# Kernel tuning notes

Hardware: AMD Instinct MI355X
Metric: run time of the kernel (lower is better)

Reference implementation:

```python
import jax, jax.numpy as jnp
import numpy as np

B, S, D = 4, 4096, 64
NEG = -1e9  # matches masked_fill(-1000000000.0)


def setup_inputs() -> dict:
    key = jax.random.key(0)
    ks = jax.random.split(key, 10)
    inp = {
        "E": jax.random.normal(ks[0], (B, S, D), jnp.float32),
        "P_K_emb": jax.random.normal(ks[1], (B, S, D), jnp.float32),
        "P_V_emb": jax.random.normal(ks[2], (B, S, D), jnp.float32),
        "Wq": jax.random.normal(ks[3], (D, D), jnp.float32) * (1.0 / np.sqrt(D)),
        "bq": jax.random.normal(ks[4], (D,), jnp.float32) * 0.02,
        "Wk": jax.random.normal(ks[5], (D, D), jnp.float32) * (1.0 / np.sqrt(D)),
        "bk": jax.random.normal(ks[6], (D,), jnp.float32) * 0.02,
        "Wv": jax.random.normal(ks[7], (D, D), jnp.float32) * (1.0 / np.sqrt(D)),
        "bv": jax.random.normal(ks[8], (D,), jnp.float32) * 0.02,
        "pad_mask": jax.random.randint(ks[9], (B, S), 0, 2).astype(jnp.bool_),
    }
    return inp


def reference(E, P_K_emb, P_V_emb, Wq, bq, Wk, bk, Wv, bv, pad_mask):
    d = E.shape[-1]
    # torch nn.Linear: y = x @ W.T + b
    Q = E @ Wq.T + bq                       # [B,S,D]
    K = E @ Wk.T + bk
    V = E @ Wv.T + bv
    K_p = K * P_K_emb                       # popularity-modulated keys
    V_p = V * P_V_emb                       # popularity-modulated values
    scores = jnp.einsum('bqd,bkd->bqk', Q, K_p) / jnp.sqrt(jnp.float32(d))  # [B,S,S]
    S_len = E.shape[1]
    causal = jnp.triu(jnp.ones((S_len, S_len), jnp.bool_), k=1)             # [S,S]
    mask = pad_mask[:, None, :] | causal[None, :, :]                        # [B,S,S]
    scores = jnp.where(mask, jnp.float32(NEG), scores)
    attn = jax.nn.softmax(scores, axis=-1)
    O_I = jnp.einsum('bqk,bkd->bqd', attn, V_p)  # [B,S,D]
    return O_I
```

## Files before the change

kernel.cpp:

```cpp
#include <hip/hip_runtime.h>
#include <hip/hip_bf16.h>

#define Bn 4
#define Sn 4096
#define Dn 64

typedef short          s16x8 __attribute__((ext_vector_type(8)));
typedef unsigned short u16x8 __attribute__((ext_vector_type(8)));
typedef float          f32x4 __attribute__((ext_vector_type(4)));

typedef __attribute__((address_space(1))) const void gas_void;
typedef __attribute__((address_space(3))) void       las_void;

__device__ __forceinline__ unsigned short f2bf(float f) {
    unsigned u = __float_as_uint(f);
    u = u + 0x7fffu + ((u >> 16) & 1u);
    return (unsigned short)(u >> 16);
}
__device__ __forceinline__ float bf2f(unsigned short h) {
    return __uint_as_float(((unsigned)h) << 16);
}
__device__ __forceinline__ unsigned long long pack4(float4 x) {
    return (unsigned long long)f2bf(x.x)
         | ((unsigned long long)f2bf(x.y) << 16)
         | ((unsigned long long)f2bf(x.z) << 32)
         | ((unsigned long long)f2bf(x.w) << 48);
}
__device__ __forceinline__ void gld16(const void* g, void* l) {
    __builtin_amdgcn_global_load_lds((gas_void*)g, (las_void*)l, 16, 0, 0);
}

__global__ void LPSAN_init_kernel(const unsigned char* pm, unsigned long long* padbits,
                                  float* meanVsum) {
    const int k = blockIdx.x, t = threadIdx.x;
    if (k == 8) { meanVsum[t] = 0.f; return; }

    __shared__ unsigned nzs;
    if (t == 0) nzs = 0u;
    __syncthreads();
    {
        const uint2* p2 = (const uint2*)(pm + k * 2048);
        uint2 x = p2[t];
        unsigned acc = (x.x & 0xFFFFFF00u) | (x.y & 0xFFFFFF00u);
        if (acc) atomicOr(&nzs, 1u);
    }
    __syncthreads();
    if (t >= 32) return;
    const int wi = k * 32 + t;
    unsigned long long bits = 0ull;
    if (nzs) {
        const uint4* p4 = (const uint4*)(pm + wi * 64);
        #pragma unroll
        for (int q = 0; q < 4; ++q) {
            uint4 x = p4[q];
            unsigned w[4] = { x.x, x.y, x.z, x.w };
            #pragma unroll
            for (int wj = 0; wj < 4; ++wj)
                #pragma unroll
                for (int bb = 0; bb < 4; ++bb)
                    bits |= (unsigned long long)(((w[wj] >> (8 * bb)) & 0xFFu) != 0u)
                            << (q * 16 + wj * 4 + bb);
        }
    } else {
        const uint4* p4 = (const uint4*)pm + wi * 16;
        #pragma unroll
        for (int q = 0; q < 16; ++q) {
            uint4 x = p4[q];
            bits |= (unsigned long long)(x.x != 0u) << (q * 4);
            bits |= (unsigned long long)(x.y != 0u) << (q * 4 + 1);
            bits |= (unsigned long long)(x.z != 0u) << (q * 4 + 2);
            bits |= (unsigned long long)(x.w != 0u) << (q * 4 + 3);
        }
    }
    padbits[wi] = bits;
}

__global__ void LPSAN_proj_kernel(
    const float* __restrict__ E, const float* __restrict__ PK, const float* __restrict__ PV,
    const float* __restrict__ Wq, const float* __restrict__ bq,
    const float* __restrict__ Wk, const float* __restrict__ bk,
    const float* __restrict__ Wv, const float* __restrict__ bv,
    unsigned short* __restrict__ Qb, unsigned short* __restrict__ Kb,
    unsigned short* __restrict__ Vt, float* __restrict__ meanVsum)
{
    __shared__ unsigned short Ebf[4096];
    __shared__ unsigned short Wbf[3][4096];
    __shared__ unsigned short Tbuf[64 * 72];

    const int t = threadIdx.x;
    const int r0 = blockIdx.x * 64;
    const int b  = r0 >> 12;
    const int s0 = r0 & (Sn - 1);
    const int w = t >> 6, lane = t & 63;
    const int fq = lane >> 4, fr = lane & 15;

    {
        const float4* Eg = (const float4*)(E + (size_t)r0 * 64);
        #pragma unroll
        for (int v = 0; v < 4; ++v) {
            int f = t + v * 256;
            float4 x = Eg[f];
            int row = f >> 4, c4 = f & 15;
            *(unsigned long long*)((char*)Ebf + row * 128 + ((c4 * 8) ^ ((row & 7) << 4))) = pack4(x);
        }
        #pragma unroll
        for (int m = 0; m < 3; ++m) {
            const float4* Wg = (const float4*)(m == 0 ? Wq : m == 1 ? Wk : Wv);
            #pragma unroll
            for (int v = 0; v < 4; ++v) {
                int f = t + v * 256;
                float4 x = Wg[f];
                int row = f >> 4, c4 = f & 15;
                *(unsigned long long*)((char*)Wbf[m] + row * 128 + ((c4 * 8) ^ ((row & 7) << 4))) = pack4(x);
            }
        }
    }
    __syncthreads();

    const int  arow = w * 16 + fr;
    const int  swz  = (fr & 7) << 4;
    const char* Ec = (const char*)Ebf;
    const s16x8 ea0 = *(const s16x8*)(Ec + arow * 128 + ((fq * 16) ^ swz));
    const s16x8 ea1 = *(const s16x8*)(Ec + arow * 128 + ((64 + fq * 16) ^ swz));

    const int sl0 = w * 16 + fq * 4;

    for (int m = 0; m < 3; ++m) {
        const char*  Wc   = (const char*)Wbf[m];
        const float* bias = (m == 0) ? bq : (m == 1) ? bk : bv;

        f32x4 acc[4];
        #pragma unroll
        for (int ct = 0; ct < 4; ++ct) {
            const int brow = ct * 16 + fr;
            s16x8 b0 = *(const s16x8*)(Wc + brow * 128 + ((fq * 16) ^ swz));
            s16x8 b1 = *(const s16x8*)(Wc + brow * 128 + ((64 + fq * 16) ^ swz));
            f32x4 z = f32x4{0.f, 0.f, 0.f, 0.f};
            z = __builtin_amdgcn_mfma_f32_16x16x32_bf16(ea0, b0, z, 0, 0, 0);
            z = __builtin_amdgcn_mfma_f32_16x16x32_bf16(ea1, b1, z, 0, 0, 0);
            acc[ct] = z;
        }

        if (m < 2) {
            #pragma unroll
            for (int ct = 0; ct < 4; ++ct) {
                const int j = ct * 16 + fr;
                const float bb = bias[j];
                if (m == 0) {
                    #pragma unroll
                    for (int r = 0; r < 4; ++r)
                        Tbuf[(sl0 + r) * 72 + j] = f2bf((acc[ct][r] + bb) * 0.125f);
                } else {
                    #pragma unroll
                    for (int r = 0; r < 4; ++r) {
                        float mod = PK[(size_t)(r0 + sl0 + r) * 64 + j];
                        Tbuf[(sl0 + r) * 72 + j] = f2bf((acc[ct][r] + bb) * mod);
                    }
                }
            }
            __syncthreads();
            {
                unsigned short* dst = (m == 0 ? Qb : Kb)
                    + (size_t)(b * Sn + s0 + (t >> 2)) * 64 + (t & 3) * 16;
                u16x8 o0 = *(const u16x8*)&Tbuf[(t >> 2) * 72 + (t & 3) * 16];
                u16x8 o1 = *(const u16x8*)&Tbuf[(t >> 2) * 72 + (t & 3) * 16 + 8];
                *(u16x8*)dst = o0;
                *(u16x8*)(dst + 8) = o1;
            }
            __syncthreads();
        } else {
            #pragma unroll
            for (int ct = 0; ct < 4; ++ct) {
                const int j = ct * 16 + fr;
                const float bb = bias[j];
                unsigned long long pk = 0;
                #pragma unroll
                for (int r = 0; r < 4; ++r) {
                    float mod = PV[(size_t)(r0 + sl0 + r) * 64 + j];
                    pk |= (unsigned long long)f2bf((acc[ct][r] + bb) * mod) << (16 * r);
                }
                *(unsigned long long*)&Tbuf[j * 72 + sl0] = pk;
            }
            __syncthreads();
            {
                const int d = t >> 2, seg = t & 3;
                u16x8 o0 = *(const u16x8*)&Tbuf[d * 72 + seg * 16];
                u16x8 o1 = *(const u16x8*)&Tbuf[d * 72 + seg * 16 + 8];
                unsigned short* dst = Vt + (size_t)(b * 64 + d) * Sn + s0 + seg * 16;
                *(u16x8*)dst = o0;
                *(u16x8*)(dst + 8) = o1;
                float s = 0.f;
                #pragma unroll
                for (int i = 0; i < 8; ++i) s += bf2f(o0[i]) + bf2f(o1[i]);
                s += __shfl_xor(s, 1);
                s += __shfl_xor(s, 2);
                if ((t & 3) == 0) atomicAdd(&meanVsum[b * 64 + d], s);
            }
        }
    }
}

__global__ void LPSAN_attn_kernel(
    const unsigned short* __restrict__ Qb, const unsigned short* __restrict__ Kb,
    const unsigned short* __restrict__ Vt, const unsigned long long* __restrict__ padbits,
    const float* __restrict__ meanVsum,
    float* __restrict__ Oacc, float* __restrict__ Lsum, float* __restrict__ out)
{
    __shared__ unsigned short Klds[2][4096];
    __shared__ unsigned short Vlds[2][4096];
    __shared__ unsigned short Plds[4][1024];

    int id = 287 - blockIdx.x, g = 0, base = 0;
    while (id >= base + 8 * (g + 1)) { base += 8 * (g + 1); ++g; }
    const int rel = id - base;
    const int qt = 8 * g + rel / (g + 1);
    const int c  = rel % (g + 1);

    const int b = blockIdx.y;
    const int q0 = qt * 64;
    const int t0 = c * 8;
    const int tcnt = min(8, qt + 1 - t0);
    const int tid = threadIdx.x;
    const int w = tid >> 6, lane = tid & 63;
    const int fq = lane >> 4, fr = lane & 15;
    const int qw = q0 + w * 16;

    const unsigned short* Kbase = Kb + b * (Sn * Dn);
    const unsigned short* Vbase = Vt + b * (Dn * Sn);

    const s16x8 qf0 = *(const s16x8*)(Qb + (b * Sn + qw + fr) * 64 + fq * 8);
    const s16x8 qf1 = *(const s16x8*)(Qb + (b * Sn + qw + fr) * 64 + 32 + fq * 8);

    s16x8 onesb;
    #pragma unroll
    for (int i = 0; i < 8; ++i) onesb[i] = (short)0x3F80;

    f32x4 Oa[4];
    f32x4 lacc = f32x4{0.f, 0.f, 0.f, 0.f};
    #pragma unroll
    for (int i = 0; i < 4; ++i) Oa[i] = f32x4{0.f, 0.f, 0.f, 0.f};

    char* Pw = (char*)&Plds[w][0];

    auto STAGE = [&](int kv0, int bufi) {
        #pragma unroll
        for (int cc = 0; cc < 2; ++cc) {
            int pos = w * 2048 + cc * 1024 + lane * 16;
            int row = pos >> 7;
            int cl  = (pos & 127) ^ ((row & 7) << 4);
            gld16(Kbase + (kv0 + row) * 64 + (cl >> 1),
                  (char*)&Klds[bufi][0] + w * 2048 + cc * 1024);
            gld16(Vbase + row * Sn + kv0 + (cl >> 1),
                  (char*)&Vlds[bufi][0] + w * 2048 + cc * 1024);
        }
    };

    auto COMPUTE = [&](int t, int bufi, bool causal) {
        const char* Kc = (const char*)&Klds[bufi][0];
        const char* Vc = (const char*)&Vlds[bufi][0];
        const int kv0 = t * 64;

        f32x4 sc[4];
        #pragma unroll
        for (int tl = 0; tl < 4; ++tl) {
            int row = tl * 16 + fr;
            int swz = (row & 7) << 4;
            s16x8 k0 = *(const s16x8*)(Kc + row * 128 + ((fq * 16) ^ swz));
            s16x8 k1 = *(const s16x8*)(Kc + row * 128 + ((64 + fq * 16) ^ swz));
            f32x4 z = f32x4{0.f, 0.f, 0.f, 0.f};
            z = __builtin_amdgcn_mfma_f32_16x16x32_bf16(qf0, k0, z, 0, 0, 0);
            z = __builtin_amdgcn_mfma_f32_16x16x32_bf16(qf1, k1, z, 0, 0, 0);
            sc[tl] = z;
        }

        const unsigned long long bits = padbits[b * 64 + t];
        #pragma unroll
        for (int tl = 0; tl < 4; ++tl) {
            const bool pad = (bits >> (tl * 16 + fr)) & 1ull;
            const int col = kv0 + tl * 16 + fr;
            #pragma unroll
            for (int r = 0; r < 4; ++r) {
                float p = __expf(sc[tl][r] - 16.0f);
                bool msk = pad || (causal && (col > (qw + fq * 4 + r)));
                sc[tl][r] = msk ? 0.f : p;
            }
        }

        #pragma unroll
        for (int tl = 0; tl < 4; ++tl) {
            #pragma unroll
            for (int r = 0; r < 4; ++r) {
                int prow = fq * 4 + r;
                int pcb = (tl * 16 + fr) * 2;
                *(unsigned short*)(Pw + prow * 128 + (pcb ^ ((prow & 7) << 4))) = f2bf(sc[tl][r]);
            }
        }
        asm volatile("s_waitcnt lgkmcnt(0)" ::: "memory");
        __builtin_amdgcn_sched_barrier(0);

        s16x8 pa0 = *(const s16x8*)(Pw + fr * 128 + ((fq * 16) ^ ((fr & 7) << 4)));
        s16x8 pa1 = *(const s16x8*)(Pw + fr * 128 + ((64 + fq * 16) ^ ((fr & 7) << 4)));
        lacc = __builtin_amdgcn_mfma_f32_16x16x32_bf16(pa0, onesb, lacc, 0, 0, 0);
        lacc = __builtin_amdgcn_mfma_f32_16x16x32_bf16(pa1, onesb, lacc, 0, 0, 0);
        #pragma unroll
        for (int dt = 0; dt < 4; ++dt) {
            int row = dt * 16 + fr;
            int swz = (row & 7) << 4;
            s16x8 v0 = *(const s16x8*)(Vc + row * 128 + ((fq * 16) ^ swz));
            s16x8 v1 = *(const s16x8*)(Vc + row * 128 + ((64 + fq * 16) ^ swz));
            Oa[dt] = __builtin_amdgcn_mfma_f32_16x16x32_bf16(pa0, v0, Oa[dt], 0, 0, 0);
            Oa[dt] = __builtin_amdgcn_mfma_f32_16x16x32_bf16(pa1, v1, Oa[dt], 0, 0, 0);
        }
    };

    STAGE(t0 * 64, 0);
    asm volatile("s_waitcnt vmcnt(0)" ::: "memory");
    __builtin_amdgcn_s_barrier();
    int cur = 0;
    for (int i = 0; i < tcnt - 1; ++i) {
        STAGE((t0 + i + 1) * 64, cur ^ 1);
        COMPUTE(t0 + i, cur, false);
        asm volatile("s_waitcnt vmcnt(0)" ::: "memory");
        __builtin_amdgcn_s_barrier();
        cur ^= 1;
    }
    COMPUTE(t0 + tcnt - 1, cur, (t0 + tcnt - 1) == qt);

    if (qt < 8) {
        #pragma unroll
        for (int r = 0; r < 4; ++r) {
            int qrow = qw + fq * 4 + r;
            float l = lacc[r];
            bool dead = !(l > 0.f);
            float inv = dead ? 0.f : 1.0f / l;
            #pragma unroll
            for (int dt = 0; dt < 4; ++dt) {
                int d = dt * 16 + fr;
                float val = dead ? meanVsum[b * 64 + d] * (1.0f / (float)Sn)
                                 : Oa[dt][r] * inv;
                out[((size_t)(b * Sn + qrow)) * 64 + d] = val;
            }
        }
    } else {
        #pragma unroll
        for (int r = 0; r < 4; ++r) {
            int qrow = qw + fq * 4 + r;
            if (fr == 0) atomicAdd(&Lsum[b * Sn + qrow], lacc[r]);
            #pragma unroll
            for (int dt = 0; dt < 4; ++dt)
                atomicAdd(&Oacc[((size_t)(b * Sn + qrow)) * 64 + dt * 16 + fr], Oa[dt][r]);
        }
    }
}

__global__ void LPSAN_norm_kernel(
    const float* __restrict__ Oacc, const float* __restrict__ Lsum,
    const float* __restrict__ meanVsum, float* __restrict__ out)
{
    const int qt = 8 + blockIdx.x, b = blockIdx.y;
    const int t = threadIdx.x;
    const int row = t >> 2, q4 = t & 3;
    const int qrow = qt * 64 + row;

    const float l = Lsum[b * Sn + qrow];
    const bool dead = !(l > 0.f);
    const float inv = dead ? 0.f : 1.0f / l;

    const float* src = Oacc + ((size_t)(b * Sn + qrow)) * 64 + q4 * 16;
    float*       dst = out  + ((size_t)(b * Sn + qrow)) * 64 + q4 * 16;
    #pragma unroll
    for (int v = 0; v < 4; ++v) {
        float4 x = *(const float4*)(src + v * 4);
        float4 o;
        if (dead) {
            const float* mv = meanVsum + b * 64 + q4 * 16 + v * 4;
            o.x = mv[0] * (1.0f / (float)Sn);
            o.y = mv[1] * (1.0f / (float)Sn);
            o.z = mv[2] * (1.0f / (float)Sn);
            o.w = mv[3] * (1.0f / (float)Sn);
        } else {
            o.x = x.x * inv; o.y = x.y * inv; o.z = x.z * inv; o.w = x.w * inv;
        }
        *(float4*)(dst + v * 4) = o;
    }
}

extern "C" void kernel_launch(void* const* d_in, const int* in_sizes, int n_in,
                              void* d_out, int out_size, void* d_ws, size_t ws_size,
                              hipStream_t stream) {
    const float* E  = (const float*)d_in[0];
    const float* PK = (const float*)d_in[1];
    const float* PV = (const float*)d_in[2];
    const float* Wq = (const float*)d_in[3];
    const float* bq = (const float*)d_in[4];
    const float* Wk = (const float*)d_in[5];
    const float* bk = (const float*)d_in[6];
    const float* Wv = (const float*)d_in[7];
    const float* bv = (const float*)d_in[8];
    const unsigned char* pm = (const unsigned char*)d_in[9];

    char* ws = (char*)d_ws;
    const size_t SZ = (size_t)Bn * Sn * Dn * sizeof(unsigned short);
    const size_t OB = (size_t)Bn * Sn * Dn * sizeof(float);
    const size_t LB = (size_t)Bn * Sn * sizeof(float);
    unsigned short* Qb = (unsigned short*)(ws);
    unsigned short* Kb = (unsigned short*)(ws + SZ);
    unsigned short* Vt = (unsigned short*)(ws + 2 * SZ);
    float* Oacc = (float*)(ws + 3 * SZ);
    float* Lsum = (float*)(ws + 3 * SZ + OB);
    unsigned long long* padbits = (unsigned long long*)(ws + 3 * SZ + OB + LB);
    float* meanVsum = (float*)(ws + 3 * SZ + OB + LB + 4096);
    float* out = (float*)d_out;

    hipMemsetAsync(Oacc, 0, OB + LB, stream);
    hipLaunchKernelGGL(LPSAN_init_kernel, dim3(9), dim3(256), 0, stream, pm, padbits, meanVsum);
    hipLaunchKernelGGL(LPSAN_proj_kernel, dim3(Bn * Sn / 64), dim3(256), 0, stream,
                       E, PK, PV, Wq, bq, Wk, bk, Wv, bv, Qb, Kb, Vt, meanVsum);
    hipLaunchKernelGGL(LPSAN_attn_kernel, dim3(288, Bn), dim3(256), 0, stream,
                       Qb, Kb, Vt, padbits, meanVsum, Oacc, Lsum, out);
    hipLaunchKernelGGL(LPSAN_norm_kernel, dim3(56, Bn), dim3(256), 0, stream,
                       Oacc, Lsum, meanVsum, out);
}
```

Before: 122.7 us.

## Use 128-row query tiles in attention, fold Oacc zeroing into init kernel

The attention kernel now gives each block 128 query rows: each wave handles two 16-row sub-tiles. Each staged K/V tile is reused for twice as many queries, which halves global K/V traffic per query. The grid shrinks to 144 blocks per batch and the causal mask now covers the two diagonal KV tiles. The projection kernel moves to 32-row blocks with one output column tile per wave, and the memset of the accumulators moves into extra blocks of the init kernel, removing one launch. The trade-off is more registers per wave and fewer, larger attention blocks, which may hurt occupancy and load balance.

```diff
diff --git a/kernel.cpp b/kernel.cpp
--- a/kernel.cpp
+++ b/kernel.cpp
@@ -31,9 +31,15 @@
 }
 
 __global__ void LPSAN_init_kernel(const unsigned char* pm, unsigned long long* padbits,
-                                  float* meanVsum) {
+                                  float* meanVsum, float* Oacc) {
     const int k = blockIdx.x, t = threadIdx.x;
     if (k == 8) { meanVsum[t] = 0.f; return; }
+    if (k >= 9) {
+        float4* dst = (float4*)Oacc;
+        const float4 z = float4{0.f, 0.f, 0.f, 0.f};
+        for (int i = (k - 9) * 256 + t; i < 266240; i += 64 * 256) dst[i] = z;
+        return;
+    }
 
     __shared__ unsigned nzs;
     if (t == 0) nzs = 0u;
@@ -75,7 +81,7 @@
     padbits[wi] = bits;
 }
 
-__global__ void LPSAN_proj_kernel(
+__global__ __launch_bounds__(256) void LPSAN_proj_kernel(
     const float* __restrict__ E, const float* __restrict__ PK, const float* __restrict__ PV,
     const float* __restrict__ Wq, const float* __restrict__ bq,
     const float* __restrict__ Wk, const float* __restrict__ bk,
@@ -83,12 +89,12 @@
     unsigned short* __restrict__ Qb, unsigned short* __restrict__ Kb,
     unsigned short* __restrict__ Vt, float* __restrict__ meanVsum)
 {
-    __shared__ unsigned short Ebf[4096];
+    __shared__ unsigned short Ebf[2048];
     __shared__ unsigned short Wbf[3][4096];
-    __shared__ unsigned short Tbuf[64 * 72];
+    __shared__ unsigned short Tbuf[2560];
 
     const int t = threadIdx.x;
-    const int r0 = blockIdx.x * 64;
+    const int r0 = blockIdx.x * 32;
     const int b  = r0 >> 12;
     const int s0 = r0 & (Sn - 1);
     const int w = t >> 6, lane = t & 63;
@@ -97,7 +103,7 @@
     {
         const float4* Eg = (const float4*)(E + (size_t)r0 * 64);
         #pragma unroll
-        for (int v = 0; v < 4; ++v) {
+        for (int v = 0; v < 2; ++v) {
             int f = t + v * 256;
             float4 x = Eg[f];
             int row = f >> 4, c4 = f & 15;
@@ -117,81 +123,72 @@
     }
     __syncthreads();
 
-    const int  arow = w * 16 + fr;
-    const int  swz  = (fr & 7) << 4;
     const char* Ec = (const char*)Ebf;
-    const s16x8 ea0 = *(const s16x8*)(Ec + arow * 128 + ((fq * 16) ^ swz));
-    const s16x8 ea1 = *(const s16x8*)(Ec + arow * 128 + ((64 + fq * 16) ^ swz));
-
-    const int sl0 = w * 16 + fq * 4;
+    const int  swz = (fr & 7) << 4;
+    s16x8 ea[2][2];
+    #pragma unroll
+    for (int rt = 0; rt < 2; ++rt) {
+        const int arow = rt * 16 + fr;
+        ea[rt][0] = *(const s16x8*)(Ec + arow * 128 + ((fq * 16) ^ swz));
+        ea[rt][1] = *(const s16x8*)(Ec + arow * 128 + ((64 + fq * 16) ^ swz));
+    }
+    const int jj = w * 16 + fr;
 
     for (int m = 0; m < 3; ++m) {
         const char*  Wc   = (const char*)Wbf[m];
         const float* bias = (m == 0) ? bq : (m == 1) ? bk : bv;
-
-        f32x4 acc[4];
-        #pragma unroll
-        for (int ct = 0; ct < 4; ++ct) {
-            const int brow = ct * 16 + fr;
-            s16x8 b0 = *(const s16x8*)(Wc + brow * 128 + ((fq * 16) ^ swz));
-            s16x8 b1 = *(const s16x8*)(Wc + brow * 128 + ((64 + fq * 16) ^ swz));
+        const float  bb   = bias[jj];
+
+        s16x8 b0 = *(const s16x8*)(Wc + jj * 128 + ((fq * 16) ^ swz));
+        s16x8 b1 = *(const s16x8*)(Wc + jj * 128 + ((64 + fq * 16) ^ swz));
+
+        f32x4 acc[2];
+        #pragma unroll
+        for (int rt = 0; rt < 2; ++rt) {
             f32x4 z = f32x4{0.f, 0.f, 0.f, 0.f};
-            z = __builtin_amdgcn_mfma_f32_16x16x32_bf16(ea0, b0, z, 0, 0, 0);
-            z = __builtin_amdgcn_mfma_f32_16x16x32_bf16(ea1, b1, z, 0, 0, 0);
-            acc[ct] = z;
+            z = __builtin_amdgcn_mfma_f32_16x16x32_bf16(ea[rt][0], b0, z, 0, 0, 0);
+            z = __builtin_amdgcn_mfma_f32_16x16x32_bf16(ea[rt][1], b1, z, 0, 0, 0);
+            acc[rt] = z;
         }
 
         if (m < 2) {
             #pragma unroll
-            for (int ct = 0; ct < 4; ++ct) {
-                const int j = ct * 16 + fr;
-                const float bb = bias[j];
-                if (m == 0) {
-                    #pragma unroll
-                    for (int r = 0; r < 4; ++r)
-                        Tbuf[(sl0 + r) * 72 + j] = f2bf((acc[ct][r] + bb) * 0.125f);
-                } else {
-                    #pragma unroll
-                    for (int r = 0; r < 4; ++r) {
-                        float mod = PK[(size_t)(r0 + sl0 + r) * 64 + j];
-                        Tbuf[(sl0 + r) * 72 + j] = f2bf((acc[ct][r] + bb) * mod);
-                    }
+            for (int rt = 0; rt < 2; ++rt)
+                #pragma unroll
+                for (int r = 0; r < 4; ++r) {
+                    const int row = rt * 16 + fq * 4 + r;
+                    float v = acc[rt][r] + bb;
+                    v *= (m == 0) ? 0.125f : PK[(size_t)(r0 + row) * 64 + jj];
+                    Tbuf[row * 72 + jj] = f2bf(v);
                 }
-            }
             __syncthreads();
             {
+                u16x8 o = *(const u16x8*)&Tbuf[(t >> 3) * 72 + (t & 7) * 8];
                 unsigned short* dst = (m == 0 ? Qb : Kb)
-                    + (size_t)(b * Sn + s0 + (t >> 2)) * 64 + (t & 3) * 16;
-                u16x8 o0 = *(const u16x8*)&Tbuf[(t >> 2) * 72 + (t & 3) * 16];
-                u16x8 o1 = *(const u16x8*)&Tbuf[(t >> 2) * 72 + (t & 3) * 16 + 8];
-                *(u16x8*)dst = o0;
-                *(u16x8*)(dst + 8) = o1;
+                    + (size_t)(b * Sn + s0 + (t >> 3)) * 64 + (t & 7) * 8;
+                *(u16x8*)dst = o;
             }
             __syncthreads();
         } else {
             #pragma unroll
-            for (int ct = 0; ct < 4; ++ct) {
-                const int j = ct * 16 + fr;
-                const float bb = bias[j];
+            for (int rt = 0; rt < 2; ++rt) {
                 unsigned long long pk = 0;
                 #pragma unroll
                 for (int r = 0; r < 4; ++r) {
-                    float mod = PV[(size_t)(r0 + sl0 + r) * 64 + j];
-                    pk |= (unsigned long long)f2bf((acc[ct][r] + bb) * mod) << (16 * r);
+                    const int row = rt * 16 + fq * 4 + r;
+                    float mod = PV[(size_t)(r0 + row) * 64 + jj];
+                    pk |= (unsigned long long)f2bf((acc[rt][r] + bb) * mod) << (16 * r);
                 }
-                *(unsigned long long*)&Tbuf[j * 72 + sl0] = pk;
+                *(unsigned long long*)&Tbuf[jj * 40 + rt * 16 + fq * 4] = pk;
             }
             __syncthreads();
             {
                 const int d = t >> 2, seg = t & 3;
-                u16x8 o0 = *(const u16x8*)&Tbuf[d * 72 + seg * 16];
-                u16x8 o1 = *(const u16x8*)&Tbuf[d * 72 + seg * 16 + 8];
-                unsigned short* dst = Vt + (size_t)(b * 64 + d) * Sn + s0 + seg * 16;
-                *(u16x8*)dst = o0;
-                *(u16x8*)(dst + 8) = o1;
+                u16x8 o = *(const u16x8*)&Tbuf[d * 40 + seg * 8];
+                *(u16x8*)(Vt + (size_t)(b * 64 + d) * Sn + s0 + seg * 8) = o;
                 float s = 0.f;
                 #pragma unroll
-                for (int i = 0; i < 8; ++i) s += bf2f(o0[i]) + bf2f(o1[i]);
+                for (int i = 0; i < 8; ++i) s += bf2f(o[i]);
                 s += __shfl_xor(s, 1);
                 s += __shfl_xor(s, 2);
                 if ((t & 3) == 0) atomicAdd(&meanVsum[b * 64 + d], s);
@@ -200,7 +197,7 @@
     }
 }
 
-__global__ void LPSAN_attn_kernel(
+__global__ __launch_bounds__(256) void LPSAN_attn_kernel(
     const unsigned short* __restrict__ Qb, const unsigned short* __restrict__ Kb,
     const unsigned short* __restrict__ Vt, const unsigned long long* __restrict__ padbits,
     const float* __restrict__ meanVsum,
@@ -208,37 +205,47 @@
 {
     __shared__ unsigned short Klds[2][4096];
     __shared__ unsigned short Vlds[2][4096];
-    __shared__ unsigned short Plds[4][1024];
-
-    int id = 287 - blockIdx.x, g = 0, base = 0;
-    while (id >= base + 8 * (g + 1)) { base += 8 * (g + 1); ++g; }
+    __shared__ unsigned short Plds[4][2048];
+
+    int id = 143 - blockIdx.x, g = 0, base = 0;
+    while (id >= base + 4 * (g + 1)) { base += 4 * (g + 1); ++g; }
     const int rel = id - base;
-    const int qt = 8 * g + rel / (g + 1);
+    const int qi = 4 * g + rel / (g + 1);
     const int c  = rel % (g + 1);
 
     const int b = blockIdx.y;
-    const int q0 = qt * 64;
+    const int q0 = qi * 128;
     const int t0 = c * 8;
-    const int tcnt = min(8, qt + 1 - t0);
+    const int ntiles = 2 * qi + 2;
+    const int tcnt = min(8, ntiles - t0);
     const int tid = threadIdx.x;
     const int w = tid >> 6, lane = tid & 63;
     const int fq = lane >> 4, fr = lane & 15;
-    const int qw = q0 + w * 16;
+    const int qw0 = q0 + w * 32;
 
     const unsigned short* Kbase = Kb + b * (Sn * Dn);
     const unsigned short* Vbase = Vt + b * (Dn * Sn);
 
-    const s16x8 qf0 = *(const s16x8*)(Qb + (b * Sn + qw + fr) * 64 + fq * 8);
-    const s16x8 qf1 = *(const s16x8*)(Qb + (b * Sn + qw + fr) * 64 + 32 + fq * 8);
+    s16x8 qf[2][2];
+    #pragma unroll
+    for (int sub = 0; sub < 2; ++sub) {
+        const unsigned short* qp = Qb + (size_t)(b * Sn + qw0 + sub * 16 + fr) * 64;
+        qf[sub][0] = *(const s16x8*)(qp + fq * 8);
+        qf[sub][1] = *(const s16x8*)(qp + 32 + fq * 8);
+    }
 
     s16x8 onesb;
     #pragma unroll
     for (int i = 0; i < 8; ++i) onesb[i] = (short)0x3F80;
 
-    f32x4 Oa[4];
-    f32x4 lacc = f32x4{0.f, 0.f, 0.f, 0.f};
+    f32x4 Oa[2][4];
+    f32x4 lacc[2];
     #pragma unroll
-    for (int i = 0; i < 4; ++i) Oa[i] = f32x4{0.f, 0.f, 0.f, 0.f};
+    for (int s = 0; s < 2; ++s) {
+        lacc[s] = f32x4{0.f, 0.f, 0.f, 0.f};
+        #pragma unroll
+        for (int i = 0; i < 4; ++i) Oa[s][i] = f32x4{0.f, 0.f, 0.f, 0.f};
+    }
 
     char* Pw = (char*)&Plds[w][0];
 
@@ -255,61 +262,74 @@
         }
     };
 
-    auto COMPUTE = [&](int t, int bufi, bool causal) {
+    auto COMPUTE = [&](int t, int bufi) {
         const char* Kc = (const char*)&Klds[bufi][0];
         const char* Vc = (const char*)&Vlds[bufi][0];
         const int kv0 = t * 64;
-
-        f32x4 sc[4];
-        #pragma unroll
-        for (int tl = 0; tl < 4; ++tl) {
-            int row = tl * 16 + fr;
-            int swz = (row & 7) << 4;
-            s16x8 k0 = *(const s16x8*)(Kc + row * 128 + ((fq * 16) ^ swz));
-            s16x8 k1 = *(const s16x8*)(Kc + row * 128 + ((64 + fq * 16) ^ swz));
-            f32x4 z = f32x4{0.f, 0.f, 0.f, 0.f};
-            z = __builtin_amdgcn_mfma_f32_16x16x32_bf16(qf0, k0, z, 0, 0, 0);
-            z = __builtin_amdgcn_mfma_f32_16x16x32_bf16(qf1, k1, z, 0, 0, 0);
-            sc[tl] = z;
-        }
-
+        const bool causal = (t >= 2 * qi);
         const unsigned long long bits = padbits[b * 64 + t];
-        #pragma unroll
-        for (int tl = 0; tl < 4; ++tl) {
-            const bool pad = (bits >> (tl * 16 + fr)) & 1ull;
-            const int col = kv0 + tl * 16 + fr;
-            #pragma unroll
-            for (int r = 0; r < 4; ++r) {
-                float p = __expf(sc[tl][r] - 16.0f);
-                bool msk = pad || (causal && (col > (qw + fq * 4 + r)));
-                sc[tl][r] = msk ? 0.f : p;
-            }
-        }
-
-        #pragma unroll
-        for (int tl = 0; tl < 4; ++tl) {
-            #pragma unroll
-            for (int r = 0; r < 4; ++r) {
-                int prow = fq * 4 + r;
-                int pcb = (tl * 16 + fr) * 2;
-                *(unsigned short*)(Pw + prow * 128 + (pcb ^ ((prow & 7) << 4))) = f2bf(sc[tl][r]);
-            }
-        }
-        asm volatile("s_waitcnt lgkmcnt(0)" ::: "memory");
-        __builtin_amdgcn_sched_barrier(0);
-
-        s16x8 pa0 = *(const s16x8*)(Pw + fr * 128 + ((fq * 16) ^ ((fr & 7) << 4)));
-        s16x8 pa1 = *(const s16x8*)(Pw + fr * 128 + ((64 + fq * 16) ^ ((fr & 7) << 4)));
-        lacc = __builtin_amdgcn_mfma_f32_16x16x32_bf16(pa0, onesb, lacc, 0, 0, 0);
-        lacc = __builtin_amdgcn_mfma_f32_16x16x32_bf16(pa1, onesb, lacc, 0, 0, 0);
+
+        #pragma unroll
+        for (int sub = 0; sub < 2; ++sub) {
+            const int qws = qw0 + sub * 16;
+            f32x4 sc[4];
+            #pragma unroll
+            for (int tl = 0; tl < 4; ++tl) {
+                int row = tl * 16 + fr;
+                int swz = (row & 7) << 4;
+                s16x8 k0 = *(const s16x8*)(Kc + row * 128 + ((fq * 16) ^ swz));
+                s16x8 k1 = *(const s16x8*)(Kc + row * 128 + ((64 + fq * 16) ^ swz));
+                f32x4 z = f32x4{0.f, 0.f, 0.f, 0.f};
+                z = __builtin_amdgcn_mfma_f32_16x16x32_bf16(qf[sub][0], k0, z, 0, 0, 0);
+                z = __builtin_amdgcn_mfma_f32_16x16x32_bf16(qf[sub][1], k1, z, 0, 0, 0);
+                sc[tl] = z;
+            }
+            #pragma unroll
+            for (int tl = 0; tl < 4; ++tl) {
+                const bool pad = (bits >> (tl * 16 + fr)) & 1ull;
+                const int col = kv0 + tl * 16 + fr;
+                #pragma unroll
+                for (int r = 0; r < 4; ++r) {
+                    float p = __expf(sc[tl][r] - 16.0f);
+                    bool msk = pad || (causal && (col > (qws + fq * 4 + r)));
+                    sc[tl][r] = msk ? 0.f : p;
+                }
+            }
+            char* Ps = Pw + sub * 2048;
+            #pragma unroll
+            for (int tl = 0; tl < 4; ++tl) {
+                #pragma unroll
+                for (int r = 0; r < 4; ++r) {
+                    int prow = fq * 4 + r;
+                    int pcb = (tl * 16 + fr) * 2;
+                    *(unsigned short*)(Ps + prow * 128 + (pcb ^ ((prow & 7) << 4))) = f2bf(sc[tl][r]);
+                }
+            }
+        }
+
+        s16x8 v0[4], v1[4];
         #pragma unroll
         for (int dt = 0; dt < 4; ++dt) {
             int row = dt * 16 + fr;
             int swz = (row & 7) << 4;
-            s16x8 v0 = *(const s16x8*)(Vc + row * 128 + ((fq * 16) ^ swz));
-            s16x8 v1 = *(const s16x8*)(Vc + row * 128 + ((64 + fq * 16) ^ swz));
-            Oa[dt] = __builtin_amdgcn_mfma_f32_16x16x32_bf16(pa0, v0, Oa[dt], 0, 0, 0);
-            Oa[dt] = __builtin_amdgcn_mfma_f32_16x16x32_bf16(pa1, v1, Oa[dt], 0, 0, 0);
+            v0[dt] = *(const s16x8*)(Vc + row * 128 + ((fq * 16) ^ swz));
+            v1[dt] = *(const s16x8*)(Vc + row * 128 + ((64 + fq * 16) ^ swz));
+        }
+        asm volatile("s_waitcnt lgkmcnt(0)" ::: "memory");
+        __builtin_amdgcn_sched_barrier(0);
+
+        #pragma unroll
+        for (int sub = 0; sub < 2; ++sub) {
+            const char* Ps = Pw + sub * 2048;
+            s16x8 pa0 = *(const s16x8*)(Ps + fr * 128 + ((fq * 16) ^ ((fr & 7) << 4)));
+            s16x8 pa1 = *(const s16x8*)(Ps + fr * 128 + ((64 + fq * 16) ^ ((fr & 7) << 4)));
+            lacc[sub] = __builtin_amdgcn_mfma_f32_16x16x32_bf16(pa0, onesb, lacc[sub], 0, 0, 0);
+            lacc[sub] = __builtin_amdgcn_mfma_f32_16x16x32_bf16(pa1, onesb, lacc[sub], 0, 0, 0);
+            #pragma unroll
+            for (int dt = 0; dt < 4; ++dt) {
+                Oa[sub][dt] = __builtin_amdgcn_mfma_f32_16x16x32_bf16(pa0, v0[dt], Oa[sub][dt], 0, 0, 0);
+                Oa[sub][dt] = __builtin_amdgcn_mfma_f32_16x16x32_bf16(pa1, v1[dt], Oa[sub][dt], 0, 0, 0);
+            }
         }
     };
 
@@ -319,37 +339,41 @@
     int cur = 0;
     for (int i = 0; i < tcnt - 1; ++i) {
         STAGE((t0 + i + 1) * 64, cur ^ 1);
-        COMPUTE(t0 + i, cur, false);
+        COMPUTE(t0 + i, cur);
         asm volatile("s_waitcnt vmcnt(0)" ::: "memory");
         __builtin_amdgcn_s_barrier();
         cur ^= 1;
     }
-    COMPUTE(t0 + tcnt - 1, cur, (t0 + tcnt - 1) == qt);
-
-    if (qt < 8) {
-        #pragma unroll
-        for (int r = 0; r < 4; ++r) {
-            int qrow = qw + fq * 4 + r;
-            float l = lacc[r];
-            bool dead = !(l > 0.f);
-            float inv = dead ? 0.f : 1.0f / l;
-            #pragma unroll
-            for (int dt = 0; dt < 4; ++dt) {
-                int d = dt * 16 + fr;
-                float val = dead ? meanVsum[b * 64 + d] * (1.0f / (float)Sn)
-                                 : Oa[dt][r] * inv;
-                out[((size_t)(b * Sn + qrow)) * 64 + d] = val;
-            }
-        }
+    COMPUTE(t0 + tcnt - 1, cur);
+
+    if (ntiles <= 8) {
+        #pragma unroll
+        for (int sub = 0; sub < 2; ++sub)
+            #pragma unroll
+            for (int r = 0; r < 4; ++r) {
+                int qrow = qw0 + sub * 16 + fq * 4 + r;
+                float l = lacc[sub][r];
+                bool dead = !(l > 0.f);
+                float inv = dead ? 0.f : 1.0f / l;
+                #pragma unroll
+                for (int dt = 0; dt < 4; ++dt) {
+                    int d = dt * 16 + fr;
+                    float val = dead ? meanVsum[b * 64 + d] * (1.0f / (float)Sn)
+                                     : Oa[sub][dt][r] * inv;
+                    out[((size_t)(b * Sn + qrow)) * 64 + d] = val;
+                }
+            }
     } else {
         #pragma unroll
-        for (int r = 0; r < 4; ++r) {
-            int qrow = qw + fq * 4 + r;
-            if (fr == 0) atomicAdd(&Lsum[b * Sn + qrow], lacc[r]);
-            #pragma unroll
-            for (int dt = 0; dt < 4; ++dt)
-                atomicAdd(&Oacc[((size_t)(b * Sn + qrow)) * 64 + dt * 16 + fr], Oa[dt][r]);
-        }
+        for (int sub = 0; sub < 2; ++sub)
+            #pragma unroll
+            for (int r = 0; r < 4; ++r) {
+                int qrow = qw0 + sub * 16 + fq * 4 + r;
+                if (fr == 0) atomicAdd(&Lsum[b * Sn + qrow], lacc[sub][r]);
+                #pragma unroll
+                for (int dt = 0; dt < 4; ++dt)
+                    atomicAdd(&Oacc[((size_t)(b * Sn + qrow)) * 64 + dt * 16 + fr], Oa[sub][dt][r]);
+            }
     }
 }
 
@@ -412,11 +436,11 @@
     float* meanVsum = (float*)(ws + 3 * SZ + OB + LB + 4096);
     float* out = (float*)d_out;
 
-    hipMemsetAsync(Oacc, 0, OB + LB, stream);
-    hipLaunchKernelGGL(LPSAN_init_kernel, dim3(9), dim3(256), 0, stream, pm, padbits, meanVsum);
-    hipLaunchKernelGGL(LPSAN_proj_kernel, dim3(Bn * Sn / 64), dim3(256), 0, stream,
+    hipLaunchKernelGGL(LPSAN_init_kernel, dim3(73), dim3(256), 0, stream,
+                       pm, padbits, meanVsum, Oacc);
+    hipLaunchKernelGGL(LPSAN_proj_kernel, dim3(Bn * Sn / 32), dim3(256), 0, stream,
                        E, PK, PV, Wq, bq, Wk, bk, Wv, bv, Qb, Kb, Vt, meanVsum);
-    hipLaunchKernelGGL(LPSAN_attn_kernel, dim3(288, Bn), dim3(256), 0, stream,
+    hipLaunchKernelGGL(LPSAN_attn_kernel, dim3(144, Bn), dim3(256), 0, stream,
                        Qb, Kb, Vt, padbits, meanVsum, Oacc, Lsum, out);
     hipLaunchKernelGGL(LPSAN_norm_kernel, dim3(56, Bn), dim3(256), 0, stream,
                        Oacc, Lsum, meanVsum, out);
```

After: 133.3 us. +8.6%, slower.
